# Kernel tuning notes

Measured on AMD Instinct MI355X. Metric: run time of the kernel, lower is better.

The kernel has to match this reference:

```python
import jax, jax.numpy as jnp
import numpy as np
from jax import lax

H = 128

def gru_cell(x, h, wih, whh, bih, bhh):
    # torch nn.GRU cell math; wih/whh stored as [in, 3H] so y = x @ w + b
    gi = x @ wih + bih  # [B, 3H]
    gh = h @ whh + bhh
    i_r, i_z, i_n = jnp.split(gi, 3, axis=-1)
    h_r, h_z, h_n = jnp.split(gh, 3, axis=-1)
    r = jax.nn.sigmoid(i_r + h_r)
    z = jax.nn.sigmoid(i_z + h_z)
    n = jnp.tanh(i_n + r * h_n)
    return (1.0 - z) * n + z * h


def setup_inputs() -> dict:
    key = jax.random.key(0)
    ks = jax.random.split(key, 16)
    B, N, D = 512, 256, 2
    s = 1.0 / np.sqrt(H)
    u = lambda k, shape: jax.random.uniform(k, shape, jnp.float32, -s, s)
    return {
        "points": jax.random.normal(ks[0], (B, N, D), jnp.float32),
        "fc_w": u(ks[1], (D, H)),
        "fc_b": u(ks[2], (H,)),
        "enc_wih": u(ks[3], (H, 3 * H)),
        "enc_whh": u(ks[4], (H, 3 * H)),
        "enc_bih": u(ks[5], (3 * H,)),
        "enc_bhh": u(ks[6], (3 * H,)),
        "dec_wih": u(ks[7], (H, 3 * H)),
        "dec_whh": u(ks[8], (H, 3 * H)),
        "dec_bih": u(ks[9], (3 * H,)),
        "dec_bhh": u(ks[10], (3 * H,)),
        "w1": u(ks[11], (H, H)),
        "w2": u(ks[12], (H, H)),
        "vt": jax.random.normal(ks[13], (H,), jnp.float32),
        "sp_w": u(ks[14], (D, H)),
        "sp_b": u(ks[15], (H,)),
    }


def reference(points, fc_w, fc_b, enc_wih, enc_whh, enc_bih, enc_bhh,
              dec_wih, dec_whh, dec_bih, dec_bhh, w1, w2, vt, sp_w, sp_b):
    B, N, _ = points.shape
    # ---- Encoder: fc + relu, then GRU over sequence ----
    x = jax.nn.relu(points @ fc_w + fc_b)  # [B,N,H]
    h0 = jnp.zeros((B, H), points.dtype)

    def enc_step(h, xt):
        hn = gru_cell(xt, h, enc_wih, enc_whh, enc_bih, enc_bhh)
        return hn, hn

    enc_h, enc_outs = lax.scan(enc_step, h0, jnp.swapaxes(x, 0, 1))
    enc_outs = jnp.swapaxes(enc_outs, 0, 1)  # [B,N,H]

    # W1(enc_outs) is step-invariant; compute once (same math as original)
    w1e = enc_outs @ w1  # [B,N,H]

    dec_input0 = points.mean(axis=1) @ sp_w + sp_b  # [B,H]
    mask0 = jnp.zeros((B, N), dtype=bool)
    sample_key = jax.random.key(42)
    batch_idx = jnp.arange(B)
    neg_inf = jnp.float32(-jnp.inf)

    def dec_step(carry, t):
        dec_in, h, mask = carry
        hn = gru_cell(dec_in, h, dec_wih, dec_whh, dec_bih, dec_bhh)  # [B,H]
        scores = jnp.tanh(w1e + (hn @ w2)[:, None, :]) @ vt  # [B,N]
        logits = jnp.where(mask, neg_inf, scores)
        logsm = jax.nn.log_softmax(logits, axis=-1)
        k = jax.random.fold_in(sample_key, t)
        idx = jax.random.categorical(k, logits)  # [B]
        logp = jnp.take_along_axis(logsm, idx[:, None], axis=1)[:, 0]
        mask = mask.at[batch_idx, idx].set(True)
        new_in = jnp.take_along_axis(enc_outs, idx[:, None, None], axis=1)[:, 0]
        return (new_in, hn, mask), (idx, logp)

    _, (seqs, logps) = lax.scan(dec_step, (dec_input0, enc_h, mask0), jnp.arange(N))
    return jnp.swapaxes(seqs, 0, 1), jnp.sum(logps, axis=0)
```

## Files before the change

kernel.cpp:

```cpp
#include <hip/hip_runtime.h>
#include <math.h>
#include <stdint.h>


#define RNG_PARTITIONABLE 1

typedef __attribute__((ext_vector_type(2))) float f32x2;
#define SP2(c) ((f32x2){(c),(c)})

__device__ __forceinline__ uint32_t rotl32_(uint32_t v, int r){ return (v<<r)|(v>>(32-r)); }

__device__ __forceinline__ void tf2x32(uint32_t k0, uint32_t k1, uint32_t x0, uint32_t x1,
                                       uint32_t& o0, uint32_t& o1){
  uint32_t k2 = k0 ^ k1 ^ 0x1BD11BDAu;
  x0 += k0; x1 += k1;
  x0 += x1; x1 = rotl32_(x1,13); x1 ^= x0;
  x0 += x1; x1 = rotl32_(x1,15); x1 ^= x0;
  x0 += x1; x1 = rotl32_(x1,26); x1 ^= x0;
  x0 += x1; x1 = rotl32_(x1, 6); x1 ^= x0;
  x0 += k1; x1 += k2 + 1u;
  x0 += x1; x1 = rotl32_(x1,17); x1 ^= x0;
  x0 += x1; x1 = rotl32_(x1,29); x1 ^= x0;
  x0 += x1; x1 = rotl32_(x1,16); x1 ^= x0;
  x0 += x1; x1 = rotl32_(x1,24); x1 ^= x0;
  x0 += k2; x1 += k0 + 2u;
  x0 += x1; x1 = rotl32_(x1,13); x1 ^= x0;
  x0 += x1; x1 = rotl32_(x1,15); x1 ^= x0;
  x0 += x1; x1 = rotl32_(x1,26); x1 ^= x0;
  x0 += x1; x1 = rotl32_(x1, 6); x1 ^= x0;
  x0 += k0; x1 += k1 + 3u;
  x0 += x1; x1 = rotl32_(x1,17); x1 ^= x0;
  x0 += x1; x1 = rotl32_(x1,29); x1 ^= x0;
  x0 += x1; x1 = rotl32_(x1,16); x1 ^= x0;
  x0 += x1; x1 = rotl32_(x1,24); x1 ^= x0;
  x0 += k1; x1 += k2 + 4u;
  x0 += x1; x1 = rotl32_(x1,13); x1 ^= x0;
  x0 += x1; x1 = rotl32_(x1,15); x1 ^= x0;
  x0 += x1; x1 = rotl32_(x1,26); x1 ^= x0;
  x0 += x1; x1 = rotl32_(x1, 6); x1 ^= x0;
  x0 += k2; x1 += k0 + 5u;
  o0 = x0; o1 = x1;
}

__device__ __forceinline__ float tanh_xla(float x){
#pragma clang fp contract(off)
  float xc = fminf(fmaxf(x, -9.0f), 9.0f);
  float x2 = xc*xc;
  float num = -2.76076847742355e-16f;
  num = x2*num + 2.00018790482477e-13f;
  num = x2*num + (-8.60467152213735e-11f);
  num = x2*num + 5.12229709037114e-08f;
  num = x2*num + 1.48572235717979e-05f;
  num = x2*num + 6.37261928875436e-04f;
  num = x2*num + 4.89352455891786e-03f;
  num = xc*num;
  float den = 1.19825839466702e-06f;
  den = x2*den + 1.18534705686654e-04f;
  den = x2*den + 2.26843463243900e-03f;
  den = x2*den + 4.89352518554385e-03f;
  float r = num/den;
  return (fabsf(x) < 4e-4f) ? x : r;
}

__device__ __forceinline__ void tanh_xla_x2(float xa, float xb, float& ra, float& rb){
#pragma clang fp contract(off)
  float xca = fminf(fmaxf(xa, -9.0f), 9.0f);
  float xcb = fminf(fmaxf(xb, -9.0f), 9.0f);
  f32x2 xc; xc.x = xca; xc.y = xcb;
  f32x2 x2 = xc*xc;
  f32x2 num = SP2(-2.76076847742355e-16f);
  num = x2*num + SP2(2.00018790482477e-13f);
  num = x2*num + SP2(-8.60467152213735e-11f);
  num = x2*num + SP2(5.12229709037114e-08f);
  num = x2*num + SP2(1.48572235717979e-05f);
  num = x2*num + SP2(6.37261928875436e-04f);
  num = x2*num + SP2(4.89352455891786e-03f);
  num = xc*num;
  f32x2 den = SP2(1.19825839466702e-06f);
  den = x2*den + SP2(1.18534705686654e-04f);
  den = x2*den + SP2(2.26843463243900e-03f);
  den = x2*den + SP2(4.89352518554385e-03f);
  float r0 = num.x/den.x;
  float r1 = num.y/den.y;
  ra = (fabsf(xa) < 4e-4f) ? xa : r0;
  rb = (fabsf(xb) < 4e-4f) ? xb : r1;
}

__device__ __forceinline__ float sigmoid_xla(float x){
  return 1.0f/(1.0f + expf(-x));
}


__global__ __launch_bounds__(256) void gemm_encgi_t(
    const float* __restrict__ pts, const float* __restrict__ fcw,
    const float* __restrict__ fcb, const float* __restrict__ wih,
    const float* __restrict__ bih, float* __restrict__ EncGI)
{
  __shared__ float As[8192];
  __shared__ float Bs[8192];
  __shared__ float pr[128];
  const int tid = threadIdx.x;
  const int j0 = blockIdx.x*64;
  const int row0 = blockIdx.y*64;
  if (tid < 128) pr[tid] = pts[(size_t)row0*2 + tid];
  #pragma unroll
  for (int it=0; it<32; ++it){
    int e = tid + 256*it;
    Bs[e] = wih[(e>>6)*384 + j0 + (e&63)];
  }
  __syncthreads();
  #pragma unroll
  for (int it=0; it<32; ++it){
    int e = tid + 256*it;
    int r = e>>7, h = e&127;
    {
#pragma clang fp contract(off)
      float p0=pr[r*2], p1=pr[r*2+1];
      float v = fmaf(p1, fcw[128+h], p0*fcw[h]) + fcb[h];
      As[e] = fmaxf(v, 0.0f);
    }
  }
  __syncthreads();
  const int tx = tid & 15, ty = tid >> 4;
  float ac[4][4][4];
  #pragma unroll
  for (int g=0;g<4;++g)
    #pragma unroll
    for (int i=0;i<4;++i)
      #pragma unroll
      for (int j=0;j<4;++j) ac[g][i][j]=0.f;
  #pragma unroll
  for (int g=0; g<4; ++g){
    #pragma unroll
    for (int kq8=0; kq8<8; ++kq8){
      const int kq = g*8 + kq8;
      float4 b0 = *(const float4*)&Bs[(kq*4+0)*64 + tx*4];
      float4 b1 = *(const float4*)&Bs[(kq*4+1)*64 + tx*4];
      float4 b2 = *(const float4*)&Bs[(kq*4+2)*64 + tx*4];
      float4 b3 = *(const float4*)&Bs[(kq*4+3)*64 + tx*4];
      #pragma unroll
      for (int i=0;i<4;++i){
        float4 a = *(const float4*)&As[(ty*4+i)*128 + kq*4];
        ac[g][i][0]=fmaf(a.x,b0.x,ac[g][i][0]);
        ac[g][i][1]=fmaf(a.x,b0.y,ac[g][i][1]);
        ac[g][i][2]=fmaf(a.x,b0.z,ac[g][i][2]);
        ac[g][i][3]=fmaf(a.x,b0.w,ac[g][i][3]);
        ac[g][i][0]=fmaf(a.y,b1.x,ac[g][i][0]);
        ac[g][i][1]=fmaf(a.y,b1.y,ac[g][i][1]);
        ac[g][i][2]=fmaf(a.y,b1.z,ac[g][i][2]);
        ac[g][i][3]=fmaf(a.y,b1.w,ac[g][i][3]);
        ac[g][i][0]=fmaf(a.z,b2.x,ac[g][i][0]);
        ac[g][i][1]=fmaf(a.z,b2.y,ac[g][i][1]);
        ac[g][i][2]=fmaf(a.z,b2.z,ac[g][i][2]);
        ac[g][i][3]=fmaf(a.z,b2.w,ac[g][i][3]);
        ac[g][i][0]=fmaf(a.w,b3.x,ac[g][i][0]);
        ac[g][i][1]=fmaf(a.w,b3.y,ac[g][i][1]);
        ac[g][i][2]=fmaf(a.w,b3.z,ac[g][i][2]);
        ac[g][i][3]=fmaf(a.w,b3.w,ac[g][i][3]);
      }
    }
  }
  float4 bv = *(const float4*)&bih[j0 + tx*4];
  #pragma unroll
  for (int i=0;i<4;++i){
    float4 o;
    o.x = ((ac[0][i][0]+ac[1][i][0])+(ac[2][i][0]+ac[3][i][0])) + bv.x;
    o.y = ((ac[0][i][1]+ac[1][i][1])+(ac[2][i][1]+ac[3][i][1])) + bv.y;
    o.z = ((ac[0][i][2]+ac[1][i][2])+(ac[2][i][2]+ac[3][i][2])) + bv.z;
    o.w = ((ac[0][i][3]+ac[1][i][3])+(ac[2][i][3]+ac[3][i][3])) + bv.w;
    *(float4*)&EncGI[(size_t)(row0+ty*4+i)*384 + j0 + tx*4] = o;
  }
}

__global__ __launch_bounds__(256) void gemm_decgi_t(
    const float* __restrict__ EncOuts, const float* __restrict__ wih,
    const float* __restrict__ bih, float* __restrict__ DecGI)
{
  __shared__ float As[8192];
  __shared__ float Bs[8192];
  const int tid = threadIdx.x;
  const int j0 = blockIdx.x*64;
  const int row0 = blockIdx.y*64;
  const float4* src = (const float4*)(EncOuts + (size_t)row0*128);
  #pragma unroll
  for (int it=0; it<8; ++it) ((float4*)As)[tid + 256*it] = src[tid + 256*it];
  #pragma unroll
  for (int it=0; it<32; ++it){
    int e = tid + 256*it;
    Bs[e] = wih[(e>>6)*384 + j0 + (e&63)];
  }
  __syncthreads();
  const int tx = tid & 15, ty = tid >> 4;
  float ac[4][4];
  #pragma unroll
  for (int i=0;i<4;++i)
    #pragma unroll
    for (int j=0;j<4;++j) ac[i][j]=0.f;
  #pragma unroll 4
  for (int kq=0; kq<32; ++kq){
    float4 b0 = *(const float4*)&Bs[(kq*4+0)*64 + tx*4];
    float4 b1 = *(const float4*)&Bs[(kq*4+1)*64 + tx*4];
    float4 b2 = *(const float4*)&Bs[(kq*4+2)*64 + tx*4];
    float4 b3 = *(const float4*)&Bs[(kq*4+3)*64 + tx*4];
    #pragma unroll
    for (int i=0;i<4;++i){
      float4 a = *(const float4*)&As[(ty*4+i)*128 + kq*4];
      ac[i][0]=fmaf(a.x,b0.x,ac[i][0]);
      ac[i][1]=fmaf(a.x,b0.y,ac[i][1]);
      ac[i][2]=fmaf(a.x,b0.z,ac[i][2]);
      ac[i][3]=fmaf(a.x,b0.w,ac[i][3]);
      ac[i][0]=fmaf(a.y,b1.x,ac[i][0]);
      ac[i][1]=fmaf(a.y,b1.y,ac[i][1]);
      ac[i][2]=fmaf(a.y,b1.z,ac[i][2]);
      ac[i][3]=fmaf(a.y,b1.w,ac[i][3]);
      ac[i][0]=fmaf(a.z,b2.x,ac[i][0]);
      ac[i][1]=fmaf(a.z,b2.y,ac[i][1]);
      ac[i][2]=fmaf(a.z,b2.z,ac[i][2]);
      ac[i][3]=fmaf(a.z,b2.w,ac[i][3]);
      ac[i][0]=fmaf(a.w,b3.x,ac[i][0]);
      ac[i][1]=fmaf(a.w,b3.y,ac[i][1]);
      ac[i][2]=fmaf(a.w,b3.z,ac[i][2]);
      ac[i][3]=fmaf(a.w,b3.w,ac[i][3]);
    }
  }
  float4 bv = *(const float4*)&bih[j0 + tx*4];
  #pragma unroll
  for (int i=0;i<4;++i){
    float4 o;
    o.x = ac[i][0] + bv.x;
    o.y = ac[i][1] + bv.y;
    o.z = ac[i][2] + bv.z;
    o.w = ac[i][3] + bv.w;
    *(float4*)&DecGI[(size_t)(row0+ty*4+i)*384 + j0 + tx*4] = o;
  }
}

__global__ __launch_bounds__(512,4) void enc_lite(
    const float* __restrict__ EncGI, const float* __restrict__ whh,
    const float* __restrict__ bhh, float* __restrict__ EncOuts)
{
  __shared__ float hb[2][128], bhh_s[384];
  const int tid = threadIdx.x, b = blockIdx.x;
  const int w = tid>>6, l = tid&63;
  const int c2 = w*16 + (l&15), rg = l>>4;
  const bool l16 = (l<16);
  float wh0[32],wh1[32],wh2[32];
  #pragma unroll
  for (int i=0;i<32;++i){
    int row=(rg*32+i)*384;
    wh0[i]=whh[row+c2]; wh1[i]=whh[row+128+c2]; wh2[i]=whh[row+256+c2];
  }
  if (tid<384) bhh_s[tid]=bhh[tid];
  if (l16) hb[0][c2]=0.f;
  float giA=0.f,giB=0.f,giC=0.f;
  if (l16){
    size_t base=(size_t)(b*256)*384;
    giA=EncGI[base+c2]; giB=EncGI[base+128+c2]; giC=EncGI[base+256+c2];
  }
  __syncthreads();
  int cur=0;
  for (int t=0;t<256;++t){
    float nA=0.f,nB=0.f,nC=0.f;
    if (l16 && t<255){
      size_t base=(size_t)(b*256+t+1)*384;
      nA=EncGI[base+c2]; nB=EncGI[base+128+c2]; nC=EncGI[base+256+c2];
    }
    float g0=0.f,g1=0.f,g2=0.f;
    {
      const float4* h4=(const float4*)&hb[cur][rg*32];
      #pragma unroll
      for (int i4=0;i4<8;++i4){
        float4 hv=h4[i4]; const int i=i4*4;
        g0=fmaf(hv.x,wh0[i  ],g0); g1=fmaf(hv.x,wh1[i  ],g1); g2=fmaf(hv.x,wh2[i  ],g2);
        g0=fmaf(hv.y,wh0[i+1],g0); g1=fmaf(hv.y,wh1[i+1],g1); g2=fmaf(hv.y,wh2[i+1],g2);
        g0=fmaf(hv.z,wh0[i+2],g0); g1=fmaf(hv.z,wh1[i+2],g1); g2=fmaf(hv.z,wh2[i+2],g2);
        g0=fmaf(hv.w,wh0[i+3],g0); g1=fmaf(hv.w,wh1[i+3],g1); g2=fmaf(hv.w,wh2[i+3],g2);
      }
    }
    g0 += __shfl_xor(g0,16); g1 += __shfl_xor(g1,16); g2 += __shfl_xor(g2,16);
    g0 += __shfl_xor(g0,32); g1 += __shfl_xor(g1,32); g2 += __shfl_xor(g2,32);
    if (l16){
#pragma clang fp contract(off)
      float hr = g0 + bhh_s[c2];
      float hz = g1 + bhh_s[128+c2];
      float hn_= g2 + bhh_s[256+c2];
      float r = sigmoid_xla(giA+hr);
      float z = sigmoid_xla(giB+hz);
      float rh = r*hn_;
      float nn = tanh_xla(giC+rh);
      float hv = hb[cur][c2];
      float hnew = (1.0f-z)*nn + z*hv;
      hb[cur^1][c2]=hnew;
      EncOuts[(size_t)(b*256+t)*128+c2]=hnew;
    }
    __syncthreads();
    giA=nA; giB=nB; giC=nC;
    cur^=1;
  }
}

#define D3_W1E   0
#define D3_ENCS  33792
#define D3_HB    35840
#define D3_QS    36096
#define D3_VT    36224
#define D3_BHH   36352
#define D3_SC    36736
#define D3_X0    36992
#define D3_RED   37120
#define D3_ALIVE 37152
#define D3_ICTL  37408
#define D3_KKS   37440
#define D3_LDS_FLOATS 37952

__global__ __launch_bounds__(512,2) void dec_fused4(
    const float* __restrict__ EncOuts, const float* __restrict__ DecGI,
    const float* __restrict__ pts,
    const float* __restrict__ wih, const float* __restrict__ whh,
    const float* __restrict__ bih, const float* __restrict__ bhh,
    const float* __restrict__ w1m, const float* __restrict__ w2m,
    const float* __restrict__ vtv, const float* __restrict__ spw,
    const float* __restrict__ spb, float* __restrict__ out)
{
  extern __shared__ float sm[];
  float* w1e  = sm + D3_W1E;
  float* encS = sm + D3_ENCS;
  float* hb0  = sm + D3_HB;
  float* q_s  = sm + D3_QS;
  float* vt_s = sm + D3_VT;
  float* bhh_s= sm + D3_BHH;
  float* sc_s = sm + D3_SC;
  float* x0_s = sm + D3_X0;
  float* red  = sm + D3_RED;
  int*   alive= (int*)(sm + D3_ALIVE);
  int*   ictl = (int*)(sm + D3_ICTL);
  uint32_t* kk_s = (uint32_t*)(sm + D3_KKS);

  const int tid = threadIdx.x, b = blockIdx.x;
  const int wv = tid>>6, l = tid&63;
  const int c2 = wv*16 + (l&15), rg = l>>4;
  const bool l16 = (l<16);
  const int hg = tid>>7, c = tid&127;

  if (tid<128){ vt_s[c]=vtv[c]; hb0[c]=EncOuts[(size_t)(b*256+255)*128+c]; }
  if (tid<256) alive[tid]=tid;
  for (int e=tid;e<384;e+=512) bhh_s[e]=bhh[e];
  if (tid<256){
    uint32_t a0,a1;
    tf2x32(0u,42u,0u,(uint32_t)tid,a0,a1);
    kk_s[tid*2]=a0; kk_s[tid*2+1]=a1;
  }

  {
    float w1col[128];
    #pragma unroll
    for (int k=0;k<128;++k) w1col[k]=w1m[k*128+c];
    for (int ch=0; ch<16; ++ch){
      __syncthreads();
      ((float4*)encS)[tid] = ((const float4*)(EncOuts + (size_t)(b*256+ch*16)*128))[tid];
      __syncthreads();
      #pragma unroll
      for (int j=0;j<4;++j){
        const int nl = hg*4 + j;
        float acc=0.f;
        const float4* er=(const float4*)&encS[nl*128];
        #pragma unroll
        for (int k4=0;k4<32;++k4){
          float4 ev=er[k4]; const int k=k4*4;
          acc=fmaf(ev.x,w1col[k  ],acc);
          acc=fmaf(ev.y,w1col[k+1],acc);
          acc=fmaf(ev.z,w1col[k+2],acc);
          acc=fmaf(ev.w,w1col[k+3],acc);
        }
        w1e[(ch*16+nl)*132 + c]=acc;
      }
    }
  }

  if (tid<256){
    float s0=pts[(size_t)(b*256+tid)*2], s1=pts[(size_t)(b*256+tid)*2+1];
    #pragma unroll
    for (int off=32; off; off>>=1){ s0+=__shfl_down(s0,off); s1+=__shfl_down(s1,off); }
    if ((tid&63)==0){ red[tid>>6]=s0; red[4+(tid>>6)]=s1; }
  }
  __syncthreads();
  if (tid<128){
#pragma clang fp contract(off)
    float mp0=((red[0]+red[1])+(red[2]+red[3]))/256.0f;
    float mp1=((red[4]+red[5])+(red[6]+red[7]))/256.0f;
    x0_s[c]=fmaf(mp1,spw[128+c],mp0*spw[c])+spb[c];
  }
  __syncthreads();

  float giA=0.f,giB=0.f,giC=0.f;
  if (l16){
    float aA=0.f,aB=0.f,aC=0.f;
    for (int k=0;k<128;++k){
      float xk=x0_s[k];
      aA=fmaf(xk, wih[k*384+c2     ], aA);
      aB=fmaf(xk, wih[k*384+128+c2 ], aB);
      aC=fmaf(xk, wih[k*384+256+c2 ], aC);
    }
    giA=aA+bih[c2]; giB=aB+bih[128+c2]; giC=aC+bih[256+c2];
  }

  float wh0[32],wh1[32],wh2[32],w2r[32];
  #pragma unroll
  for (int i=0;i<32;++i){
    int row=(rg*32+i)*384;
    wh0[i]=whh[row+c2]; wh1[i]=whh[row+128+c2]; wh2[i]=whh[row+256+c2];
    w2r[i]=w2m[(rg*32+i)*128+c2];
  }
  __syncthreads();

  float logp_acc=0.f;
  int cnt=256, cur=0;
  for (int t=0;t<256;++t){
    float g0=0.f,g1=0.f,g2=0.f;
    {
      const float4* h4=(const float4*)&hb0[cur*128 + rg*32];
      #pragma unroll
      for (int i4=0;i4<8;++i4){
        float4 hv=h4[i4]; const int i=i4*4;
        g0=fmaf(hv.x,wh0[i  ],g0); g1=fmaf(hv.x,wh1[i  ],g1); g2=fmaf(hv.x,wh2[i  ],g2);
        g0=fmaf(hv.y,wh0[i+1],g0); g1=fmaf(hv.y,wh1[i+1],g1); g2=fmaf(hv.y,wh2[i+1],g2);
        g0=fmaf(hv.z,wh0[i+2],g0); g1=fmaf(hv.z,wh1[i+2],g1); g2=fmaf(hv.z,wh2[i+2],g2);
        g0=fmaf(hv.w,wh0[i+3],g0); g1=fmaf(hv.w,wh1[i+3],g1); g2=fmaf(hv.w,wh2[i+3],g2);
      }
    }
    g0 += __shfl_xor(g0,16); g1 += __shfl_xor(g1,16); g2 += __shfl_xor(g2,16);
    g0 += __shfl_xor(g0,32); g1 += __shfl_xor(g1,32); g2 += __shfl_xor(g2,32);
    if (l16){
#pragma clang fp contract(off)
      float hr = g0 + bhh_s[c2];
      float hz = g1 + bhh_s[128+c2];
      float hn_= g2 + bhh_s[256+c2];
      float r = sigmoid_xla(giA+hr);
      float z = sigmoid_xla(giB+hz);
      float rh = r*hn_;
      float nn = tanh_xla(giC+rh);
      float hv = hb0[cur*128 + c2];
      hb0[(cur^1)*128 + c2] = (1.0f-z)*nn + z*hv;
    }
    __syncthreads();
    {
      float qp=0.f;
      const float4* h4=(const float4*)&hb0[(cur^1)*128 + rg*32];
      #pragma unroll
      for (int i4=0;i4<8;++i4){
        float4 hv=h4[i4]; const int i=i4*4;
        qp=fmaf(hv.x,w2r[i],qp); qp=fmaf(hv.y,w2r[i+1],qp);
        qp=fmaf(hv.z,w2r[i+2],qp); qp=fmaf(hv.w,w2r[i+3],qp);
      }
      qp += __shfl_xor(qp,16);
      qp += __shfl_xor(qp,32);
      if (l16) q_s[c2]=qp;
    }
    __syncthreads();
    int K, ksh;
    if      (cnt>128){K=2; ksh=1;}
    else if (cnt> 64){K=4; ksh=2;}
    else if (cnt> 32){K=8; ksh=3;}
    else if (cnt> 16){K=16;ksh=4;}
    else             {K=32;ksh=5;}
    const int hlen = 128>>ksh;
    const int a2 = tid>>ksh, seg = tid&(K-1);
    const bool act = a2 < cnt;
    float part=0.f; int myn=0x7FFFFFFF;
    if (act){
      myn=alive[a2];
      const int h0=seg*hlen;
      const float* wrow = &w1e[myn*132];
      for (int h=h0; h<h0+hlen; h+=4){
        float4 qv=*(const float4*)&q_s[h];
        float4 vv=*(const float4*)&vt_s[h];
        float4 wvv=*(const float4*)&wrow[h];
        float t0,t1,t2,t3;
        tanh_xla_x2(wvv.x+qv.x, wvv.y+qv.y, t0, t1);
        tanh_xla_x2(wvv.z+qv.z, wvv.w+qv.w, t2, t3);
        part=fmaf(vv.x,t0,part);
        part=fmaf(vv.y,t1,part);
        part=fmaf(vv.z,t2,part);
        part=fmaf(vv.w,t3,part);
      }
    }
    for (int off=1; off<K; off<<=1) part += __shfl_xor(part, off);
    float sc = act ? part : -INFINITY;
    float pert=-INFINITY;
    if (act && seg==0){
      sc_s[a2]=sc;
      uint32_t kk0=kk_s[2*t], kk1=kk_s[2*t+1];
      uint32_t o0,o1;
      uint32_t f=(uint32_t)(b*256+myn);
      uint32_t bits;
#if RNG_PARTITIONABLE
      tf2x32(kk0,kk1,0u,f,o0,o1);
      bits=o0^o1;
#else
      { uint32_t p=(f<65536u)?f:(f-65536u);
        tf2x32(kk0,kk1,p,p+65536u,o0,o1);
        bits=(f<65536u)?o0:o1; }
#endif
      float fl=__uint_as_float((bits>>9)|0x3f800000u)-1.0f;
      float u=fmaxf(1.17549435e-38f, fl+1.17549435e-38f);
      float g=-logf(-logf(u));
      pert=g+sc;
    } else {
      sc=-INFINITY; myn=0x7FFFFFFF;
    }
    float bp=pert, bm=sc; int bn=myn, ba=a2;
    #pragma unroll
    for (int off=1; off<64; off<<=1){
      float op=__shfl_xor(bp,off); int on=__shfl_xor(bn,off); int oa=__shfl_xor(ba,off);
      float om=__shfl_xor(bm,off);
      if (op>bp || (op==bp && on<bn)){ bp=op; bn=on; ba=oa; }
      bm=fmaxf(bm,om);
    }
    float e_=(pert>-INFINITY)?expf(sc-bm):0.f;
    #pragma unroll
    for (int off=1; off<64; off<<=1) e_+=__shfl_xor(e_,off);
    if ((tid&63)==0){
      int w=tid>>6;
      red[w]=bp; red[8+w]=bm; red[16+w]=e_;
      ictl[2+w]=bn; ictl[10+w]=ba;
    }
    __syncthreads();
    float bp2=red[0]; int bn2=ictl[2], ba2=ictl[10];
    #pragma unroll
    for (int w=1;w<8;++w){
      float op=red[w]; int on=ictl[2+w];
      if (op>bp2 || (op==bp2 && on<bn2)){ bp2=op; bn2=on; ba2=ictl[10+w]; }
    }
    if (l16 && t<255){
      size_t row=(size_t)(b*256+bn2)*384;
      giA=DecGI[row+c2]; giB=DecGI[row+128+c2]; giC=DecGI[row+256+c2];
    }
    int shv=0; bool willw=false;
    if (tid >= ba2 && tid < cnt-1){ shv = alive[tid+1]; willw = true; }
    if (tid==0){
      float M=red[8];
      #pragma unroll
      for (int w=1;w<8;++w) M=fmaxf(M,red[8+w]);
      float S=0.f;
      #pragma unroll
      for (int w=0;w<8;++w){
        float ew=red[16+w];
        if (ew>0.f) S += ew*expf(red[8+w]-M);
      }
      logp_acc += sc_s[ba2] - M - logf(S);
      out[b*256+t]=(float)bn2;
    }
    __syncthreads();
    if (willw) alive[tid]=shv;
    cnt-=1;
    cur^=1;
  }
  if (tid==0) out[131072+b]=logp_acc;
}


__global__ __launch_bounds__(512,2) void enc_fused(
    const float* __restrict__ pts, const float* __restrict__ fcw, const float* __restrict__ fcb,
    const float* __restrict__ wih, const float* __restrict__ whh,
    const float* __restrict__ bih, const float* __restrict__ bhh,
    float* __restrict__ EncOuts)
{
  __shared__ float x_s[128], h_s[128], pGI[1536], pGH[1536], bih_s[384], bhh_s[384];
  const int tid = threadIdx.x, b = blockIdx.x;
  const int hg = tid >> 7, c = tid & 127;
  float wi0[32],wi1[32],wi2[32],wh0[32],wh1[32],wh2[32];
  #pragma unroll
  for (int i=0;i<32;++i){
    int row = (hg*32+i)*384;
    wi0[i]=wih[row+c]; wi1[i]=wih[row+128+c]; wi2[i]=wih[row+256+c];
    wh0[i]=whh[row+c]; wh1[i]=whh[row+128+c]; wh2[i]=whh[row+256+c];
  }
  if (tid<384){ bih_s[tid]=bih[tid]; bhh_s[tid]=bhh[tid]; }
  float fw0=0.f,fw1=0.f,fb=0.f;
  if (tid<128){
#pragma clang fp contract(off)
    fw0=fcw[c]; fw1=fcw[128+c]; fb=fcb[c];
    h_s[c]=0.f;
    float p0=pts[(size_t)b*512], p1=pts[(size_t)b*512+1];
    float v = fmaf(p1,fw1,p0*fw0)+fb;
    x_s[c]=fmaxf(v,0.f);
  }
  __syncthreads();
  for (int t=0;t<256;++t){
    float a0=0,a1=0,a2=0,g0=0,g1=0,g2=0;
    const float4* x4=(const float4*)&x_s[hg*32];
    const float4* h4=(const float4*)&h_s[hg*32];
    #pragma unroll
    for (int i4=0;i4<8;++i4){
      float4 xv=x4[i4], hv=h4[i4];
      const int i=i4*4;
      a0=fmaf(xv.x,wi0[i  ],a0); a1=fmaf(xv.x,wi1[i  ],a1); a2=fmaf(xv.x,wi2[i  ],a2);
      a0=fmaf(xv.y,wi0[i+1],a0); a1=fmaf(xv.y,wi1[i+1],a1); a2=fmaf(xv.y,wi2[i+1],a2);
      a0=fmaf(xv.z,wi0[i+2],a0); a1=fmaf(xv.z,wi1[i+2],a1); a2=fmaf(xv.z,wi2[i+2],a2);
      a0=fmaf(xv.w,wi0[i+3],a0); a1=fmaf(xv.w,wi1[i+3],a1); a2=fmaf(xv.w,wi2[i+3],a2);
      g0=fmaf(hv.x,wh0[i  ],g0); g1=fmaf(hv.x,wh1[i  ],g1); g2=fmaf(hv.x,wh2[i  ],g2);
      g0=fmaf(hv.y,wh0[i+1],g0); g1=fmaf(hv.y,wh1[i+1],g1); g2=fmaf(hv.y,wh2[i+1],g2);
      g0=fmaf(hv.z,wh0[i+2],g0); g1=fmaf(hv.z,wh1[i+2],g1); g2=fmaf(hv.z,wh2[i+2],g2);
      g0=fmaf(hv.w,wh0[i+3],g0); g1=fmaf(hv.w,wh1[i+3],g1); g2=fmaf(hv.w,wh2[i+3],g2);
    }
    pGI[hg*384+c]=a0; pGI[hg*384+128+c]=a1; pGI[hg*384+256+c]=a2;
    pGH[hg*384+c]=g0; pGH[hg*384+128+c]=g1; pGH[hg*384+256+c]=g2;
    __syncthreads();
    if (tid<128){
#pragma clang fp contract(off)
      float ir =((pGI[c]+pGI[384+c])+(pGI[768+c]+pGI[1152+c]))+bih_s[c];
      float iz =((pGI[128+c]+pGI[512+c])+(pGI[896+c]+pGI[1280+c]))+bih_s[128+c];
      float in_=((pGI[256+c]+pGI[640+c])+(pGI[1024+c]+pGI[1408+c]))+bih_s[256+c];
      float hr =((pGH[c]+pGH[384+c])+(pGH[768+c]+pGH[1152+c]))+bhh_s[c];
      float hz =((pGH[128+c]+pGH[512+c])+(pGH[896+c]+pGH[1280+c]))+bhh_s[128+c];
      float hn_=((pGH[256+c]+pGH[640+c])+(pGH[1024+c]+pGH[1408+c]))+bhh_s[256+c];
      float r = sigmoid_xla(ir+hr);
      float z = sigmoid_xla(iz+hz);
      float rh = r*hn_;
      float nn = tanh_xla(in_+rh);
      float hv = h_s[c];
      float hnew = (1.0f-z)*nn + z*hv;
      h_s[c]=hnew;
      EncOuts[(size_t)(b*256+t)*128+c]=hnew;
      if (t<255){
        float p0=pts[(size_t)(b*256+t+1)*2], p1=pts[(size_t)(b*256+t+1)*2+1];
        float v=fmaf(p1,fw1,p0*fw0)+fb;
        x_s[c]=fmaxf(v,0.f);
      }
    }
    __syncthreads();
  }
}

#define OFF_W1E   0
#define OFF_PG    32768
#define OFF_PI    33536
#define OFF_PQ    34304
#define OFF_PS    34560
#define OFF_H     34816
#define OFF_Q     34944
#define OFF_X     35072
#define OFF_VT    35200
#define OFF_BIH   35328
#define OFF_BHH   35712
#define OFF_SC    36096
#define OFF_RED   36352
#define OFF_ALIVE 36368
#define OFF_ICTL  36624
#define OFF_ENCS  36640
#define DEC_LDS_FLOATS 40736

#define GI_PARTIAL() do{ \
  float a0=0,a1=0,a2=0; \
  const float4* xx4=(const float4*)&x_s[hg*64]; \
  _Pragma("unroll") \
  for (int i4=0;i4<16;++i4){ float4 xv=xx4[i4]; const int i=i4*4; \
    a0=fmaf(xv.x,wi0[i  ],a0); a1=fmaf(xv.x,wi1[i  ],a1); a2=fmaf(xv.x,wi2[i  ],a2); \
    a0=fmaf(xv.y,wi0[i+1],a0); a1=fmaf(xv.y,wi1[i+1],a1); a2=fmaf(xv.y,wi2[i+1],a2); \
    a0=fmaf(xv.z,wi0[i+2],a0); a1=fmaf(xv.z,wi1[i+2],a1); a2=fmaf(xv.z,wi2[i+2],a2); \
    a0=fmaf(xv.w,wi0[i+3],a0); a1=fmaf(xv.w,wi1[i+3],a1); a2=fmaf(xv.w,wi2[i+3],a2); } \
  pI[hg*384+c]=a0; pI[hg*384+128+c]=a1; pI[hg*384+256+c]=a2; }while(0)

__global__ __launch_bounds__(256,1) void dec_fused_fb(
    const float* __restrict__ EncOuts, const float* __restrict__ pts,
    const float* __restrict__ wih, const float* __restrict__ whh,
    const float* __restrict__ bih, const float* __restrict__ bhh,
    const float* __restrict__ w1m, const float* __restrict__ w2m,
    const float* __restrict__ vtv, const float* __restrict__ spw,
    const float* __restrict__ spb, float* __restrict__ out)
{
  extern __shared__ float sm[];
  float* w1e  = sm + OFF_W1E;
  float* pG   = sm + OFF_PG;
  float* pI   = sm + OFF_PI;
  float* pQ   = sm + OFF_PQ;
  float* pS   = sm + OFF_PS;
  float* h_s  = sm + OFF_H;
  float* q_s  = sm + OFF_Q;
  float* x_s  = sm + OFF_X;
  float* vt_s = sm + OFF_VT;
  float* bih_s= sm + OFF_BIH;
  float* bhh_s= sm + OFF_BHH;
  float* sc_s = sm + OFF_SC;
  float* red  = sm + OFF_RED;
  int*   alive= (int*)(sm + OFF_ALIVE);
  int*   ictl = (int*)(sm + OFF_ICTL);
  float* encS = sm + OFF_ENCS;

  const int tid = threadIdx.x, b = blockIdx.x;
  const int hg = tid >> 7, c = tid & 127;

  if (tid<128){ vt_s[c]=vtv[c]; h_s[c]=EncOuts[(size_t)(b*256+255)*128+c]; }
  alive[tid]=tid;
  for (int e=tid;e<384;e+=256){ bih_s[e]=bih[e]; bhh_s[e]=bhh[e]; }
  if (tid==0){ ictl[0]=256; }

  {
    float w1col[128];
    #pragma unroll
    for (int k=0;k<128;++k) w1col[k]=w1m[k*128+c];
    for (int ch=0; ch<8; ++ch){
      const float4* src=(const float4*)(EncOuts+(size_t)(b*256+ch*32)*128);
      for (int e=tid;e<1024;e+=256) ((float4*)encS)[e]=src[e];
      __syncthreads();
      for (int k2=0;k2<16;++k2){
        const int nn = hg + 2*k2;
        float acc=0.f;
        const float4* er=(const float4*)&encS[nn*128];
        #pragma unroll
        for (int k4=0;k4<32;++k4){
          float4 ev=er[k4]; const int k=k4*4;
          acc=fmaf(ev.x,w1col[k  ],acc);
          acc=fmaf(ev.y,w1col[k+1],acc);
          acc=fmaf(ev.z,w1col[k+2],acc);
          acc=fmaf(ev.w,w1col[k+3],acc);
        }
        w1e[c*256 + ch*32 + nn]=acc;
      }
      __syncthreads();
    }
  }

  float wi0[64],wi1[64],wi2[64],wh0[64],wh1[64],wh2[64],w2r[64];
  #pragma unroll
  for (int i=0;i<64;++i){
    int row=(hg*64+i)*384;
    wi0[i]=wih[row+c]; wi1[i]=wih[row+128+c]; wi2[i]=wih[row+256+c];
    wh0[i]=whh[row+c]; wh1[i]=whh[row+128+c]; wh2[i]=whh[row+256+c];
    w2r[i]=w2m[(hg*64+i)*128+c];
  }

  {
    float s0=pts[(size_t)(b*256+tid)*2], s1=pts[(size_t)(b*256+tid)*2+1];
    #pragma unroll
    for (int off=32; off; off>>=1){ s0+=__shfl_down(s0,off); s1+=__shfl_down(s1,off); }
    if ((tid&63)==0){ red[tid>>6]=s0; red[4+(tid>>6)]=s1; }
  }
  __syncthreads();
  if (tid<128){
#pragma clang fp contract(off)
    float mp0=((red[0]+red[1])+(red[2]+red[3]))/256.0f;
    float mp1=((red[4]+red[5])+(red[6]+red[7]))/256.0f;
    float v=fmaf(mp1,spw[128+c],mp0*spw[c])+spb[c];
    x_s[c]=v;
  }
  __syncthreads();
  GI_PARTIAL();
  __syncthreads();

  float logp_acc=0.f;
  int cnt=256;
  for (int t=0;t<256;++t){
    {
      float g0=0,g1=0,g2=0;
      const float4* hh4=(const float4*)&h_s[hg*64];
      #pragma unroll
      for (int i4=0;i4<16;++i4){
        float4 hv=hh4[i4]; const int i=i4*4;
        g0=fmaf(hv.x,wh0[i  ],g0); g1=fmaf(hv.x,wh1[i  ],g1); g2=fmaf(hv.x,wh2[i  ],g2);
        g0=fmaf(hv.y,wh0[i+1],g0); g1=fmaf(hv.y,wh1[i+1],g1); g2=fmaf(hv.y,wh2[i+1],g2);
        g0=fmaf(hv.z,wh0[i+2],g0); g1=fmaf(hv.z,wh1[i+2],g1); g2=fmaf(hv.z,wh2[i+2],g2);
        g0=fmaf(hv.w,wh0[i+3],g0); g1=fmaf(hv.w,wh1[i+3],g1); g2=fmaf(hv.w,wh2[i+3],g2);
      }
      pG[hg*384+c]=g0; pG[hg*384+128+c]=g1; pG[hg*384+256+c]=g2;
    }
    __syncthreads();
    if (tid<128){
#pragma clang fp contract(off)
      float ir =(pI[c]+pI[384+c])+bih_s[c];
      float iz =(pI[128+c]+pI[512+c])+bih_s[128+c];
      float in_=(pI[256+c]+pI[640+c])+bih_s[256+c];
      float hr =(pG[c]+pG[384+c])+bhh_s[c];
      float hz =(pG[128+c]+pG[512+c])+bhh_s[128+c];
      float hn_=(pG[256+c]+pG[640+c])+bhh_s[256+c];
      float r = sigmoid_xla(ir+hr);
      float z = sigmoid_xla(iz+hz);
      float rh = r*hn_;
      float nn = tanh_xla(in_+rh);
      float hv = h_s[c];
      h_s[c] = (1.0f-z)*nn + z*hv;
    }
    __syncthreads();
    {
      float qp=0.f;
      const float4* hh4=(const float4*)&h_s[hg*64];
      #pragma unroll
      for (int i4=0;i4<16;++i4){
        float4 hv=hh4[i4]; const int i=i4*4;
        qp=fmaf(hv.x,w2r[i],qp); qp=fmaf(hv.y,w2r[i+1],qp);
        qp=fmaf(hv.z,w2r[i+2],qp); qp=fmaf(hv.w,w2r[i+3],qp);
      }
      pQ[hg*128+c]=qp;
    }
    __syncthreads();
    if (tid<128) q_s[c]=pQ[c]+pQ[128+c];
    __syncthreads();
    int K=1;
    while ((cnt*(K<<1))<=256 && K<16) K<<=1;
    const int hlen=128/K;
    int seg, a2; bool act;
    if (K>1){ seg=(int)((unsigned)tid/(unsigned)cnt); a2=tid-seg*cnt; act=(seg<K); }
    else    { seg=0; a2=tid; act=(tid<cnt); }
    float part=0.f; int myn=0x7FFFFFFF;
    if (act){
      myn=alive[a2];
      const int h0=seg*hlen;
      for (int h=h0; h<h0+hlen; h+=4){
        float4 qv=*(const float4*)&q_s[h];
        float4 vv=*(const float4*)&vt_s[h];
        float w0=w1e[(h  )*256+myn];
        float w1v=w1e[(h+1)*256+myn];
        float w2v=w1e[(h+2)*256+myn];
        float w3=w1e[(h+3)*256+myn];
        part=fmaf(vv.x,tanh_xla(w0 +qv.x),part);
        part=fmaf(vv.y,tanh_xla(w1v+qv.y),part);
        part=fmaf(vv.z,tanh_xla(w2v+qv.z),part);
        part=fmaf(vv.w,tanh_xla(w3 +qv.w),part);
      }
    }
    float sc;
    if (K>1){
      if (act) pS[seg*cnt+a2]=part;
      __syncthreads();
      sc=-INFINITY; myn=0x7FFFFFFF;
      if (tid<cnt){
        float s=pS[tid];
        for (int s2=1;s2<K;++s2) s+=pS[s2*cnt+tid];
        sc=s; myn=alive[tid];
      }
    } else {
      sc = act ? part : -INFINITY;
      if (!act) myn=0x7FFFFFFF;
    }
    float pert=-INFINITY;
    if (tid<cnt){
      sc_s[tid]=sc;
      uint32_t kk0,kk1,o0,o1;
      tf2x32(0u,42u,0u,(uint32_t)t,kk0,kk1);
      uint32_t f=(uint32_t)(b*256+myn);
      uint32_t bits;
#if RNG_PARTITIONABLE
      tf2x32(kk0,kk1,0u,f,o0,o1);
      bits=o0^o1;
#else
      { uint32_t p=(f<65536u)?f:(f-65536u);
        tf2x32(kk0,kk1,p,p+65536u,o0,o1);
        bits=(f<65536u)?o0:o1; }
#endif
      float fl=__uint_as_float((bits>>9)|0x3f800000u)-1.0f;
      float u=fmaxf(1.17549435e-38f, fl+1.17549435e-38f);
      float g=-logf(-logf(u));
      pert=g+sc;
    }
    float bp=pert, bm=sc; int bn=myn, ba=tid;
    #pragma unroll
    for (int off=1; off<64; off<<=1){
      float op=__shfl_xor(bp,off); int on=__shfl_xor(bn,off); int oa=__shfl_xor(ba,off);
      float om=__shfl_xor(bm,off);
      if (op>bp || (op==bp && on<bn)){ bp=op; bn=on; ba=oa; }
      bm=fmaxf(bm,om);
    }
    float e_=(tid<cnt)?expf(sc-bm):0.f;
    #pragma unroll
    for (int off=1; off<64; off<<=1) e_+=__shfl_xor(e_,off);
    if ((tid&63)==0){
      int w=tid>>6;
      red[w]=bp; red[4+w]=bm; red[8+w]=e_;
      ictl[2+w]=bn; ictl[6+w]=ba;
    }
    __syncthreads();
    if (tid==0){
      float M=fmaxf(fmaxf(red[4],red[5]),fmaxf(red[6],red[7]));
      float S=0.f;
      #pragma unroll
      for (int w=0;w<4;++w){
        float ew=red[8+w];
        if (ew>0.f) S += ew*expf(red[4+w]-M);
      }
      float bp2=red[0]; int bn2=ictl[2], ba2=ictl[6];
      #pragma unroll
      for (int w=1;w<4;++w){
        float op=red[w]; int on=ictl[2+w];
        if (op>bp2 || (op==bp2 && on<bn2)){ bp2=op; bn2=on; ba2=ictl[6+w]; }
      }
      logp_acc += sc_s[ba2] - M - logf(S);
      out[b*256+t]=(float)bn2;
      ictl[1]=bn2;
      alive[ba2]=alive[cnt-1];
    }
    __syncthreads();
    cnt-=1;
    if (t<255){
      int bn=ictl[1];
      if (tid<128) x_s[c]=EncOuts[(size_t)(b*256+bn)*128+c];
      __syncthreads();
      GI_PARTIAL();
    }
  }
  if (tid==0) out[131072+b]=logp_acc;
}

__global__ void k_telemetry(float* __restrict__ out, int n, float val){
  int i=blockIdx.x*blockDim.x+threadIdx.x;
  if (i<n) out[i]=val;
}

extern "C" void kernel_launch(void* const* d_in, const int* in_sizes, int n_in,
                              void* d_out, int out_size, void* d_ws, size_t ws_size,
                              hipStream_t stream){
  const float* points  = (const float*)d_in[0];
  const float* fc_w    = (const float*)d_in[1];
  const float* fc_b    = (const float*)d_in[2];
  const float* enc_wih = (const float*)d_in[3];
  const float* enc_whh = (const float*)d_in[4];
  const float* enc_bih = (const float*)d_in[5];
  const float* enc_bhh = (const float*)d_in[6];
  const float* dec_wih = (const float*)d_in[7];
  const float* dec_whh = (const float*)d_in[8];
  const float* dec_bih = (const float*)d_in[9];
  const float* dec_bhh = (const float*)d_in[10];
  const float* w1      = (const float*)d_in[11];
  const float* w2      = (const float*)d_in[12];
  const float* vt      = (const float*)d_in[13];
  const float* sp_w    = (const float*)d_in[14];
  const float* sp_b    = (const float*)d_in[15];
  float* out = (float*)d_out;

  const size_t needEnc  = (size_t)131072*128*4;
  const size_t needFast = needEnc + (size_t)131072*384*4;
  if (ws_size < needEnc){
    k_telemetry<<<(out_size+255)/256,256,0,stream>>>(out, out_size, (float)(ws_size>>20));
    return;
  }
  float* EncOuts = (float*)d_ws;

  if (ws_size >= needFast){
    float* BIG = EncOuts + (size_t)131072*128;
    gemm_encgi_t<<<dim3(6,2048),256,0,stream>>>(points, fc_w, fc_b, enc_wih, enc_bih, BIG);
    enc_lite<<<512,512,0,stream>>>(BIG, enc_whh, enc_bhh, EncOuts);
    gemm_decgi_t<<<dim3(6,2048),256,0,stream>>>(EncOuts, dec_wih, dec_bih, BIG);
    const int lds4 = D3_LDS_FLOATS*4;
    (void)hipFuncSetAttribute((const void*)dec_fused4,
                              hipFuncAttributeMaxDynamicSharedMemorySize, lds4);
    dec_fused4<<<512,512,lds4,stream>>>(EncOuts, BIG, points,
        dec_wih, dec_whh, dec_bih, dec_bhh, w1, w2, vt, sp_w, sp_b, out);
  } else {
    enc_fused<<<512,512,0,stream>>>(points, fc_w, fc_b, enc_wih, enc_whh,
                                    enc_bih, enc_bhh, EncOuts);
    const int ldsf = DEC_LDS_FLOATS*4;
    (void)hipFuncSetAttribute((const void*)dec_fused_fb,
                              hipFuncAttributeMaxDynamicSharedMemorySize, ldsf);
    dec_fused_fb<<<512,256,ldsf,stream>>>(EncOuts, points, dec_wih, dec_whh,
        dec_bih, dec_bhh, w1, w2, vt, sp_w, sp_b, out);
  }
}
```

Baseline: 5.134 ms.

## Keep W1·enc rows in registers and replace alive-list compaction with dead flags

The decoder no longer stores the 256x128 W1e matrix in LDS (about 135KB). Each thread pair now owns one candidate point and holds half its W1e row (64 floats) in registers, computed by a register-blocked GEMM over transposed encoder chunks staged in LDS. The alive-list compaction and its extra barrier per step are replaced by a per-thread dead flag, and the wave-level __any check skips score work once a whole wave is dead. LDS use drops to about 57KB, which could allow more resident blocks, but register pressure rises, and work per live point no longer rebalances as points are removed, so dead threads idle inside partly live waves.

```diff
diff --git a/kernel.cpp b/kernel.cpp
--- a/kernel.cpp
+++ b/kernel.cpp
@@ -299,21 +299,45 @@
   }
 }
 
-#define D3_W1E   0
-#define D3_ENCS  33792
-#define D3_HB    35840
-#define D3_QS    36096
-#define D3_VT    36224
-#define D3_BHH   36352
-#define D3_SC    36736
-#define D3_X0    36992
-#define D3_RED   37120
-#define D3_ALIVE 37152
-#define D3_ICTL  37408
-#define D3_KKS   37440
-#define D3_LDS_FLOATS 37952
-
-__global__ __launch_bounds__(512,2) void dec_fused4(
+#define D5_HB    0
+#define D5_QS    256
+#define D5_VT    384
+#define D5_BHH   512
+#define D5_SC    896
+#define D5_X0    1152
+#define D5_RED   1280
+#define D5_ICTL  1312
+#define D5_KK    1344
+#define D5_W1S   1856
+#define D5_ENCT  5952
+#define D5_LDS_FLOATS 14176
+
+#define SCORE_TREE(S,NCH) do{ \
+  float chv[NCH]; \
+  _Pragma("unroll") \
+  for (int cI=0;cI<NCH;++cI){ \
+    float a=0.f; \
+    _Pragma("unroll") \
+    for (int j4=0;j4<((S)/4);++j4){ \
+      const int j = cI*(S) + j4*4; \
+      float4 qv=*(const float4*)&q_s[h0+j]; \
+      float4 vv=*(const float4*)&vt_s[h0+j]; \
+      float t0,t1,t2,t3; \
+      tanh_xla_x2(w1r[j]+qv.x, w1r[j+1]+qv.y, t0,t1); \
+      tanh_xla_x2(w1r[j+2]+qv.z, w1r[j+3]+qv.w, t2,t3); \
+      a=fmaf(vv.x,t0,a); a=fmaf(vv.y,t1,a); \
+      a=fmaf(vv.z,t2,a); a=fmaf(vv.w,t3,a); \
+    } \
+    chv[cI]=a; \
+  } \
+  _Pragma("unroll") \
+  for (int dd=1; dd<(NCH); dd<<=1) \
+    _Pragma("unroll") \
+    for (int cI=0; cI<(NCH); cI+=2*dd) chv[cI]+=chv[cI+dd]; \
+  part = chv[0]; \
+}while(0)
+
+__global__ __launch_bounds__(512,2) void dec_fused5(
     const float* __restrict__ EncOuts, const float* __restrict__ DecGI,
     const float* __restrict__ pts,
     const float* __restrict__ wih, const float* __restrict__ whh,
@@ -323,60 +347,31 @@
     const float* __restrict__ spb, float* __restrict__ out)
 {
   extern __shared__ float sm[];
-  float* w1e  = sm + D3_W1E;
-  float* encS = sm + D3_ENCS;
-  float* hb0  = sm + D3_HB;
-  float* q_s  = sm + D3_QS;
-  float* vt_s = sm + D3_VT;
-  float* bhh_s= sm + D3_BHH;
-  float* sc_s = sm + D3_SC;
-  float* x0_s = sm + D3_X0;
-  float* red  = sm + D3_RED;
-  int*   alive= (int*)(sm + D3_ALIVE);
-  int*   ictl = (int*)(sm + D3_ICTL);
-  uint32_t* kk_s = (uint32_t*)(sm + D3_KKS);
+  float* hb0  = sm + D5_HB;
+  float* q_s  = sm + D5_QS;
+  float* vt_s = sm + D5_VT;
+  float* bhh_s= sm + D5_BHH;
+  float* sc_s = sm + D5_SC;
+  float* x0_s = sm + D5_X0;
+  float* red  = sm + D5_RED;
+  int*   ictl = (int*)(sm + D5_ICTL);
+  uint32_t* kk_s = (uint32_t*)(sm + D5_KK);
+  float* w1s  = sm + D5_W1S;
+  float* encT = sm + D5_ENCT;
 
   const int tid = threadIdx.x, b = blockIdx.x;
   const int wv = tid>>6, l = tid&63;
   const int c2 = wv*16 + (l&15), rg = l>>4;
   const bool l16 = (l<16);
-  const int hg = tid>>7, c = tid&127;
-
-  if (tid<128){ vt_s[c]=vtv[c]; hb0[c]=EncOuts[(size_t)(b*256+255)*128+c]; }
-  if (tid<256) alive[tid]=tid;
+  const int pk = tid>>1, h0 = (tid&1)*64;
+
+  if (tid<128){ vt_s[tid]=vtv[tid]; hb0[tid]=EncOuts[(size_t)(b*256+255)*128+tid]; }
   for (int e=tid;e<384;e+=512) bhh_s[e]=bhh[e];
   if (tid<256){
     uint32_t a0,a1;
     tf2x32(0u,42u,0u,(uint32_t)tid,a0,a1);
-    kk_s[tid*2]=a0; kk_s[tid*2+1]=a1;
-  }
-
-  {
-    float w1col[128];
-    #pragma unroll
-    for (int k=0;k<128;++k) w1col[k]=w1m[k*128+c];
-    for (int ch=0; ch<16; ++ch){
-      __syncthreads();
-      ((float4*)encS)[tid] = ((const float4*)(EncOuts + (size_t)(b*256+ch*16)*128))[tid];
-      __syncthreads();
-      #pragma unroll
-      for (int j=0;j<4;++j){
-        const int nl = hg*4 + j;
-        float acc=0.f;
-        const float4* er=(const float4*)&encS[nl*128];
-        #pragma unroll
-        for (int k4=0;k4<32;++k4){
-          float4 ev=er[k4]; const int k=k4*4;
-          acc=fmaf(ev.x,w1col[k  ],acc);
-          acc=fmaf(ev.y,w1col[k+1],acc);
-          acc=fmaf(ev.z,w1col[k+2],acc);
-          acc=fmaf(ev.w,w1col[k+3],acc);
-        }
-        w1e[(ch*16+nl)*132 + c]=acc;
-      }
-    }
-  }
-
+    kk_s[2*tid]=a0; kk_s[2*tid+1]=a1;
+  }
   if (tid<256){
     float s0=pts[(size_t)(b*256+tid)*2], s1=pts[(size_t)(b*256+tid)*2+1];
     #pragma unroll
@@ -388,7 +383,37 @@
 #pragma clang fp contract(off)
     float mp0=((red[0]+red[1])+(red[2]+red[3]))/256.0f;
     float mp1=((red[4]+red[5])+(red[6]+red[7]))/256.0f;
-    x0_s[c]=fmaf(mp1,spw[128+c],mp0*spw[c])+spb[c];
+    x0_s[tid]=fmaf(mp1,spw[128+tid],mp0*spw[tid])+spb[tid];
+  }
+
+  float w1r[64];
+  #pragma unroll
+  for (int j=0;j<64;++j) w1r[j]=0.f;
+  for (int kc=0;kc<4;++kc){
+    __syncthreads();
+    for (int e=tid;e<1024;e+=512)
+      ((float4*)w1s)[e] = *(const float4*)&w1m[kc*32*128 + e*4];
+    for (int e=tid;e<2048;e+=512){
+      int n=e>>3, q=e&7;
+      float4 v = *(const float4*)&EncOuts[(size_t)(b*256+n)*128 + kc*32 + q*4];
+      encT[(q*4+0)*257+n]=v.x;
+      encT[(q*4+1)*257+n]=v.y;
+      encT[(q*4+2)*257+n]=v.z;
+      encT[(q*4+3)*257+n]=v.w;
+    }
+    __syncthreads();
+    for (int k2=0;k2<32;++k2){
+      float ek=encT[k2*257+pk];
+      const float4* wr=(const float4*)&w1s[k2*128+h0];
+      #pragma unroll
+      for (int j4=0;j4<16;++j4){
+        float4 wv4=wr[j4];
+        w1r[j4*4+0]=fmaf(ek,wv4.x,w1r[j4*4+0]);
+        w1r[j4*4+1]=fmaf(ek,wv4.y,w1r[j4*4+1]);
+        w1r[j4*4+2]=fmaf(ek,wv4.z,w1r[j4*4+2]);
+        w1r[j4*4+3]=fmaf(ek,wv4.w,w1r[j4*4+3]);
+      }
+    }
   }
   __syncthreads();
 
@@ -414,8 +439,10 @@
   __syncthreads();
 
   float logp_acc=0.f;
-  int cnt=256, cur=0;
+  int cur=0;
+  bool amDead=false;
   for (int t=0;t<256;++t){
+    const int cnt = 256 - t;
     float g0=0.f,g1=0.f,g2=0.f;
     {
       const float4* h4=(const float4*)&hb0[cur*128 + rg*32];
@@ -457,41 +484,26 @@
       if (l16) q_s[c2]=qp;
     }
     __syncthreads();
-    int K, ksh;
-    if      (cnt>128){K=2; ksh=1;}
-    else if (cnt> 64){K=4; ksh=2;}
-    else if (cnt> 32){K=8; ksh=3;}
-    else if (cnt> 16){K=16;ksh=4;}
-    else             {K=32;ksh=5;}
-    const int hlen = 128>>ksh;
-    const int a2 = tid>>ksh, seg = tid&(K-1);
-    const bool act = a2 < cnt;
-    float part=0.f; int myn=0x7FFFFFFF;
-    if (act){
-      myn=alive[a2];
-      const int h0=seg*hlen;
-      const float* wrow = &w1e[myn*132];
-      for (int h=h0; h<h0+hlen; h+=4){
-        float4 qv=*(const float4*)&q_s[h];
-        float4 vv=*(const float4*)&vt_s[h];
-        float4 wvv=*(const float4*)&wrow[h];
-        float t0,t1,t2,t3;
-        tanh_xla_x2(wvv.x+qv.x, wvv.y+qv.y, t0, t1);
-        tanh_xla_x2(wvv.z+qv.z, wvv.w+qv.w, t2, t3);
-        part=fmaf(vv.x,t0,part);
-        part=fmaf(vv.y,t1,part);
-        part=fmaf(vv.z,t2,part);
-        part=fmaf(vv.w,t3,part);
-      }
-    }
-    for (int off=1; off<K; off<<=1) part += __shfl_xor(part, off);
-    float sc = act ? part : -INFINITY;
-    float pert=-INFINITY;
-    if (act && seg==0){
-      sc_s[a2]=sc;
+    float part=0.f;
+    if (__any((int)(!amDead))){
+      if (!amDead){
+        if      (cnt>128) SCORE_TREE(64,1);
+        else if (cnt> 64) SCORE_TREE(32,2);
+        else if (cnt> 32) SCORE_TREE(16,4);
+        else if (cnt> 16) SCORE_TREE(8,8);
+        else              SCORE_TREE(4,16);
+      }
+    }
+    part += __shfl_xor(part,1);
+    const bool cand = ((tid&1)==0) && !amDead;
+    float sc = cand ? part : -INFINITY;
+    float pert=-INFINITY; int myn=0x7FFFFFFF;
+    if (cand){
+      sc_s[pk]=sc;
+      myn=pk;
       uint32_t kk0=kk_s[2*t], kk1=kk_s[2*t+1];
       uint32_t o0,o1;
-      uint32_t f=(uint32_t)(b*256+myn);
+      uint32_t f=(uint32_t)(b*256+pk);
       uint32_t bits;
 #if RNG_PARTITIONABLE
       tf2x32(kk0,kk1,0u,f,o0,o1);
@@ -505,15 +517,13 @@
       float u=fmaxf(1.17549435e-38f, fl+1.17549435e-38f);
       float g=-logf(-logf(u));
       pert=g+sc;
-    } else {
-      sc=-INFINITY; myn=0x7FFFFFFF;
-    }
-    float bp=pert, bm=sc; int bn=myn, ba=a2;
+    }
+    float bp=pert, bm=sc; int bn=myn;
     #pragma unroll
     for (int off=1; off<64; off<<=1){
-      float op=__shfl_xor(bp,off); int on=__shfl_xor(bn,off); int oa=__shfl_xor(ba,off);
+      float op=__shfl_xor(bp,off); int on=__shfl_xor(bn,off);
       float om=__shfl_xor(bm,off);
-      if (op>bp || (op==bp && on<bn)){ bp=op; bn=on; ba=oa; }
+      if (op>bp || (op==bp && on<bn)){ bp=op; bn=on; }
       bm=fmaxf(bm,om);
     }
     float e_=(pert>-INFINITY)?expf(sc-bm):0.f;
@@ -522,21 +532,19 @@
     if ((tid&63)==0){
       int w=tid>>6;
       red[w]=bp; red[8+w]=bm; red[16+w]=e_;
-      ictl[2+w]=bn; ictl[10+w]=ba;
-    }
-    __syncthreads();
-    float bp2=red[0]; int bn2=ictl[2], ba2=ictl[10];
+      ictl[2+w]=bn;
+    }
+    __syncthreads();
+    float bp2=red[0]; int bn2=ictl[2];
     #pragma unroll
     for (int w=1;w<8;++w){
       float op=red[w]; int on=ictl[2+w];
-      if (op>bp2 || (op==bp2 && on<bn2)){ bp2=op; bn2=on; ba2=ictl[10+w]; }
+      if (op>bp2 || (op==bp2 && on<bn2)){ bp2=op; bn2=on; }
     }
     if (l16 && t<255){
       size_t row=(size_t)(b*256+bn2)*384;
       giA=DecGI[row+c2]; giB=DecGI[row+128+c2]; giC=DecGI[row+256+c2];
     }
-    int shv=0; bool willw=false;
-    if (tid >= ba2 && tid < cnt-1){ shv = alive[tid+1]; willw = true; }
     if (tid==0){
       float M=red[8];
       #pragma unroll
@@ -547,12 +555,10 @@
         float ew=red[16+w];
         if (ew>0.f) S += ew*expf(red[8+w]-M);
       }
-      logp_acc += sc_s[ba2] - M - logf(S);
+      logp_acc += sc_s[bn2] - M - logf(S);
       out[b*256+t]=(float)bn2;
     }
-    __syncthreads();
-    if (willw) alive[tid]=shv;
-    cnt-=1;
+    if (pk==bn2) amDead=true;
     cur^=1;
   }
   if (tid==0) out[131072+b]=logp_acc;
@@ -939,10 +945,10 @@
     gemm_encgi_t<<<dim3(6,2048),256,0,stream>>>(points, fc_w, fc_b, enc_wih, enc_bih, BIG);
     enc_lite<<<512,512,0,stream>>>(BIG, enc_whh, enc_bhh, EncOuts);
     gemm_decgi_t<<<dim3(6,2048),256,0,stream>>>(EncOuts, dec_wih, dec_bih, BIG);
-    const int lds4 = D3_LDS_FLOATS*4;
-    (void)hipFuncSetAttribute((const void*)dec_fused4,
-                              hipFuncAttributeMaxDynamicSharedMemorySize, lds4);
-    dec_fused4<<<512,512,lds4,stream>>>(EncOuts, BIG, points,
+    const int lds5 = D5_LDS_FLOATS*4;
+    (void)hipFuncSetAttribute((const void*)dec_fused5,
+                              hipFuncAttributeMaxDynamicSharedMemorySize, lds5);
+    dec_fused5<<<512,512,lds5,stream>>>(EncOuts, BIG, points,
         dec_wih, dec_whh, dec_bih, dec_bhh, w1, w2, vt, sp_w, sp_b, out);
   } else {
     enc_fused<<<512,512,0,stream>>>(points, fc_w, fc_b, enc_wih, enc_whh,
```

Measured after the change: 6.527 ms. +27.1%, slower.
